# Optimization experiments

Hardware: AMD Instinct MI355X
Metric: run time of the kernel (lower is better)

Reference implementation:

```python
import jax, jax.numpy as jnp
import numpy as np
import math

HIDDEN = 768
KEY = 128      # attention_key_size
INTER = 1536   # intermediate_size
B, S = 4, 2048


def setup_inputs() -> dict:
    key = jax.random.key(0)
    ks = jax.random.split(key, 8)
    hidden_states = jax.random.normal(ks[0], (B, S, HIDDEN), dtype=jnp.float32)
    attention_mask = jax.random.randint(ks[1], (B, 1, 1, S), 0, 2, dtype=jnp.int32)
    position_ids = jnp.arange(B * S, dtype=jnp.int32).reshape(B, S) % S
    Wi = jax.random.normal(ks[2], (HIDDEN, 2 * INTER + KEY), dtype=jnp.float32) * 0.02
    bi = jnp.zeros((2 * INTER + KEY,), dtype=jnp.float32)
    gamma = jax.random.normal(ks[3], (2, KEY), dtype=jnp.float32) * 0.02 + 1.0
    beta = jnp.zeros((2, KEY), dtype=jnp.float32)
    Wo = jax.random.normal(ks[4], (INTER, HIDDEN), dtype=jnp.float32) * 0.02
    bo = jnp.zeros((HIDDEN,), dtype=jnp.float32)
    return {"hidden_states": hidden_states, "attention_mask": attention_mask,
            "position_ids": position_ids, "Wi": Wi, "bi": bi,
            "gamma": gamma, "beta": beta, "Wo": Wo, "bo": bo}


def _gau_forward(hidden_states, attention_mask, Wi, bi, gamma, beta, Wo, bo):
    # i_dense + swish activation
    h = jax.nn.silu(jnp.einsum('bsd,de->bse', hidden_states, Wi) + bi)
    u = h[..., :INTER]
    v = h[..., INTER:2 * INTER]
    qk = h[..., 2 * INTER:]
    # OffsetScale: per-head affine (heads=2 -> q, k)
    q = qk * gamma[0] + beta[0]
    k = qk * gamma[1] + beta[1]
    scores = jnp.einsum('bid,bjd->bij', q, k) / math.sqrt(KEY)
    # additive mask: (1 - m) * -1e12, squeeze head dim
    am = (1.0 - attention_mask.astype(scores.dtype)) * -1e12
    scores = scores + am[:, 0]  # [B,1,S] broadcasts over query dim
    # softmax_plus normalization: scale logits by log(l)/log(512)
    valid = (scores > -1e11).astype(scores.dtype)
    l = jnp.maximum(jnp.sum(valid, axis=-1, keepdims=True), 1.0)
    scale = jnp.log(l) / jnp.log(jnp.asarray(512.0, scores.dtype))
    attn = jax.nn.softmax(scores * scale, axis=-1)
    ctx = jnp.einsum('bij,bjd->bid', attn, v)
    return jnp.einsum('bse,eh->bsh', u * ctx, Wo) + bo


def reference(hidden_states, attention_mask, position_ids, Wi, bi, gamma, beta, Wo, bo):
    # position_ids unused: p_bias is not 'rotary'
    return _gau_forward(hidden_states, attention_mask, Wi, bi, gamma, beta, Wo, bo)
```

## Files before the change

kernel.cpp:

```cpp
#include <hip/hip_runtime.h>
#include <math.h>

#define HIDDEN 768
#define KEY    128
#define INTER  1536
#define NB     4
#define SEQ    2048
#define MTOT   (NB*SEQ)
#define ETOT   (2*INTER+KEY)
#define CS     136

typedef short bf16x8 __attribute__((ext_vector_type(8)));
typedef float f32x4  __attribute__((ext_vector_type(4)));
typedef unsigned short u16x8 __attribute__((ext_vector_type(8)));

__device__ __forceinline__ unsigned short f2bfbits(float x) {
    union { float f; unsigned int u; } a; a.f = x;
    unsigned int r = a.u + 0x7fffu + ((a.u >> 16) & 1u);
    return (unsigned short)(r >> 16);
}
__device__ __forceinline__ float bfbits2f(unsigned short b) {
    union { float f; unsigned int u; } a; a.u = ((unsigned int)b) << 16;
    return a.f;
}

__device__ __forceinline__ void gl2lds16(const unsigned short* g, unsigned short* l) {
    __builtin_amdgcn_global_load_lds(
        (const __attribute__((address_space(1))) unsigned int*)g,
        (__attribute__((address_space(3))) unsigned int*)l, 16, 0, 0);
}

__global__ __launch_bounds__(256) void scale_kernel(const int* __restrict__ mask,
                                                    float* __restrict__ scaleb) {
    __shared__ int red[256];
    int b = blockIdx.x;
    int s = 0;
    for (int j = threadIdx.x; j < SEQ; j += 256)
        s += (mask[b*SEQ + j] != 0) ? 1 : 0;
    red[threadIdx.x] = s;
    __syncthreads();
    for (int step = 128; step > 0; step >>= 1) {
        if (threadIdx.x < step) red[threadIdx.x] += red[threadIdx.x + step];
        __syncthreads();
    }
    if (threadIdx.x == 0) {
        float l = fmaxf((float)red[0], 1.0f);
        scaleb[b] = logf(l) / logf(512.0f);
    }
}

__global__ __launch_bounds__(256) void cvt_bf16_kernel(const float* __restrict__ in,
                                                       unsigned short* __restrict__ out, int n4) {
    int i = blockIdx.x*256 + threadIdx.x;
    if (i < n4) {
        float4 v = ((const float4*)in)[i];
        ushort4 o;
        o.x = f2bfbits(v.x); o.y = f2bfbits(v.y);
        o.z = f2bfbits(v.z); o.w = f2bfbits(v.w);
        ((ushort4*)out)[i] = o;
    }
}

__global__ __launch_bounds__(256) void transpose_cvt(const float* __restrict__ in,
                                                     unsigned short* __restrict__ out,
                                                     int R, int C) {
    __shared__ unsigned short tile[32][33];
    int c0 = blockIdx.x*32, r0 = blockIdx.y*32;
    int tx = threadIdx.x & 31, ty4 = (threadIdx.x >> 5)*4;
    #pragma unroll
    for (int rr = 0; rr < 4; rr++) {
        int r = ty4 + rr;
        tile[r][tx] = f2bfbits(in[(size_t)(r0+r)*C + c0+tx]);
    }
    __syncthreads();
    #pragma unroll
    for (int rr = 0; rr < 4; rr++) {
        int r = ty4 + rr;
        out[(size_t)(c0+r)*R + r0+tx] = tile[tx][r];
    }
}

__device__ __forceinline__ void mfma_core(
    const unsigned short* __restrict__ Abase, int lda,
    const unsigned short* __restrict__ Bbase, int ldb,
    unsigned short* As, unsigned short* Bs,
    f32x4 acc[4][4], int tid, int ktot)
{
    const int lane = tid & 63, wave = tid >> 6;
    const int wm = (wave >> 1) << 6, wn = (wave & 1) << 6;
    const int lm = lane & 15;
    const int q8 = (lane >> 4) << 3;
    const int row_a = tid >> 2, col_a = (tid & 3) << 3;
    const int row_b = row_a + 64;

    for (int k0 = 0; k0 < ktot; k0 += 64) {
        if (k0) __syncthreads();
        gl2lds16(Abase + (size_t)row_a*lda + k0 + col_a,        As + tid*8);
        gl2lds16(Abase + (size_t)row_b*lda + k0 + col_a,        As + (tid+256)*8);
        gl2lds16(Bbase + (size_t)row_a*ldb + k0 + col_a,        Bs + tid*8);
        gl2lds16(Bbase + (size_t)row_b*ldb + k0 + col_a,        Bs + (tid+256)*8);
        gl2lds16(Abase + (size_t)row_a*lda + k0+32 + col_a,     As + 4096 + tid*8);
        gl2lds16(Abase + (size_t)row_b*lda + k0+32 + col_a,     As + 4096 + (tid+256)*8);
        gl2lds16(Bbase + (size_t)row_a*ldb + k0+32 + col_a,     Bs + 4096 + tid*8);
        gl2lds16(Bbase + (size_t)row_b*ldb + k0+32 + col_a,     Bs + 4096 + (tid+256)*8);
        __syncthreads();
        #pragma unroll
        for (int h = 0; h < 2; h++) {
            const unsigned short* Ah = As + h*4096;
            const unsigned short* Bh = Bs + h*4096;
            bf16x8 af[4], bfr[4];
            #pragma unroll
            for (int i = 0; i < 4; i++)
                af[i] = *(const bf16x8*)&Ah[(wm + i*16 + lm)*32 + q8];
            #pragma unroll
            for (int j = 0; j < 4; j++)
                bfr[j] = *(const bf16x8*)&Bh[(wn + j*16 + lm)*32 + q8];
            #pragma unroll
            for (int i = 0; i < 4; i++)
                #pragma unroll
                for (int j = 0; j < 4; j++)
                    acc[i][j] = __builtin_amdgcn_mfma_f32_16x16x32_bf16(af[i], bfr[j], acc[i][j], 0, 0, 0);
        }
    }
}

#define EPILOG_IDX \
    const int lane = tid & 63, wave = tid >> 6; \
    const int wm = (wave >> 1) << 6, wn = (wave & 1) << 6; \
    const int cn = lane & 15, r4 = (lane >> 4) << 2;

__global__ __launch_bounds__(256) void gemm1_mfma(
    const unsigned short* __restrict__ Xb, const unsigned short* __restrict__ WiT,
    const float* __restrict__ bi, const float* __restrict__ gamma, const float* __restrict__ beta,
    unsigned short* __restrict__ u, unsigned short* __restrict__ vT,
    unsigned short* __restrict__ qb, unsigned short* __restrict__ kb)
{
    __shared__ __align__(16) unsigned short smem[128*CS];
    unsigned short* As = smem;
    unsigned short* Bs = smem + 8192;
    const int tid = threadIdx.x;
    const int row0 = blockIdx.y*128, col0 = blockIdx.x*128;
    f32x4 acc[4][4];
    #pragma unroll
    for (int i = 0; i < 4; i++)
        #pragma unroll
        for (int j = 0; j < 4; j++)
            acc[i][j] = (f32x4){0.f,0.f,0.f,0.f};
    mfma_core(Xb + (size_t)row0*HIDDEN, HIDDEN, WiT + (size_t)col0*HIDDEN, HIDDEN,
              As, Bs, acc, tid, HIDDEN);
    EPILOG_IDX
    __syncthreads();
    #pragma unroll
    for (int j = 0; j < 4; j++) {
        int nl = wn + j*16 + cn;
        float bin = bi[col0 + nl];
        #pragma unroll
        for (int i = 0; i < 4; i++) {
            #pragma unroll
            for (int r = 0; r < 4; r++) {
                int rowl = wm + i*16 + r4 + r;
                float x = acc[i][j][r] + bin;
                float h = x / (1.0f + __expf(-x));
                smem[rowl*CS + nl] = f2bfbits(h);
            }
        }
    }
    __syncthreads();
    if (col0 < INTER) {
        #pragma unroll
        for (int rnd = 0; rnd < 8; rnd++) {
            int row = rnd*16 + (tid>>4);
            int col = (tid&15)*8;
            u16x8 h = *(const u16x8*)&smem[row*CS + col];
            *(u16x8*)&u[(size_t)(row0+row)*INTER + col0 + col] = h;
        }
    } else if (col0 < 2*INTER) {
        int c = tid >> 1;
        int half = tid & 1;
        int b = row0 / SEQ;
        int srow = row0 - b*SEQ + half*64;
        size_t base = ((size_t)b*INTER + (col0 - INTER) + c)*SEQ + srow;
        #pragma unroll
        for (int k = 0; k < 8; k++) {
            u16x8 h;
            #pragma unroll
            for (int t = 0; t < 8; t++)
                h[t] = smem[(half*64 + k*8 + t)*CS + c];
            *(u16x8*)&vT[base + k*8] = h;
        }
    } else {
        #pragma unroll
        for (int rnd = 0; rnd < 8; rnd++) {
            int row = rnd*16 + (tid>>4);
            int col = (tid&15)*8;
            u16x8 h = *(const u16x8*)&smem[row*CS + col];
            int m = row0 + row;
            u16x8 qo, ko;
            #pragma unroll
            for (int t = 0; t < 8; t++) {
                float hv = bfbits2f(h[t]);
                qo[t] = f2bfbits(hv*gamma[col+t]     + beta[col+t]);
                ko[t] = f2bfbits(hv*gamma[KEY+col+t] + beta[KEY+col+t]);
            }
            *(u16x8*)&qb[(size_t)m*KEY + col] = qo;
            *(u16x8*)&kb[(size_t)m*KEY + col] = ko;
        }
    }
}

__global__ __launch_bounds__(256) void attn_mfma(
    const unsigned short* __restrict__ qb, const unsigned short* __restrict__ kb,
    const int* __restrict__ mask, const float* __restrict__ scaleb,
    unsigned short* __restrict__ P)
{
    __shared__ __align__(16) unsigned short smem[128*CS];
    unsigned short* As = smem;
    unsigned short* Bs = smem + 8192;
    const int tid = threadIdx.x;
    const int z = blockIdx.z;
    const int row0 = blockIdx.y*128, col0 = blockIdx.x*128;
    f32x4 acc[4][4];
    #pragma unroll
    for (int i = 0; i < 4; i++)
        #pragma unroll
        for (int j = 0; j < 4; j++)
            acc[i][j] = (f32x4){0.f,0.f,0.f,0.f};
    mfma_core(qb + ((size_t)z*SEQ + row0)*KEY, KEY, kb + ((size_t)z*SEQ + col0)*KEY, KEY,
              As, Bs, acc, tid, KEY);
    const float st = scaleb[z] * 0.08838834764831845f;
    EPILOG_IDX
    __syncthreads();
    #pragma unroll
    for (int j = 0; j < 4; j++) {
        int nl = wn + j*16 + cn;
        float mkf = (mask[z*SEQ + col0 + nl] != 0) ? 1.0f : 0.0f;
        #pragma unroll
        for (int i = 0; i < 4; i++) {
            #pragma unroll
            for (int r = 0; r < 4; r++) {
                int rowl = wm + i*16 + r4 + r;
                float p = mkf * __expf(acc[i][j][r]*st);
                smem[rowl*CS + nl] = f2bfbits(p);
            }
        }
    }
    __syncthreads();
    #pragma unroll
    for (int rnd = 0; rnd < 8; rnd++) {
        int row = rnd*16 + (tid>>4);
        int col = (tid&15)*8;
        u16x8 h = *(const u16x8*)&smem[row*CS + col];
        *(u16x8*)&P[((size_t)z*SEQ + row0 + row)*SEQ + col0 + col] = h;
    }
}

__global__ __launch_bounds__(256) void rowsum_kernel(const unsigned short* __restrict__ P,
                                                     float* __restrict__ lbuf) {
    int row = blockIdx.x*4 + (threadIdx.x >> 6);
    int lane = threadIdx.x & 63;
    const unsigned short* pr = P + (size_t)row*SEQ;
    float s = 0.f;
    for (int c = lane*8; c < SEQ; c += 64*8) {
        ushort4 a = *(const ushort4*)&pr[c];
        ushort4 b = *(const ushort4*)&pr[c+4];
        s += bfbits2f(a.x)+bfbits2f(a.y)+bfbits2f(a.z)+bfbits2f(a.w)
           + bfbits2f(b.x)+bfbits2f(b.y)+bfbits2f(b.z)+bfbits2f(b.w);
    }
    #pragma unroll
    for (int off = 32; off > 0; off >>= 1) s += __shfl_down(s, off, 64);
    if (lane == 0) lbuf[row] = s;
}

__global__ __launch_bounds__(256) void pv_mfma(
    const unsigned short* __restrict__ P, const unsigned short* __restrict__ vT,
    const float* __restrict__ lbuf, unsigned short* __restrict__ u)
{
    __shared__ __align__(16) unsigned short smem[128*CS];
    unsigned short* As = smem;
    unsigned short* Bs = smem + 8192;
    const int tid = threadIdx.x;
    const int z = blockIdx.z;
    const int row0 = blockIdx.y*128, col0 = blockIdx.x*128;
    f32x4 acc[4][4];
    #pragma unroll
    for (int i = 0; i < 4; i++)
        #pragma unroll
        for (int j = 0; j < 4; j++)
            acc[i][j] = (f32x4){0.f,0.f,0.f,0.f};
    mfma_core(P + ((size_t)z*SEQ + row0)*SEQ, SEQ, vT + ((size_t)z*INTER + col0)*SEQ, SEQ,
              As, Bs, acc, tid, SEQ);
    EPILOG_IDX
    __syncthreads();
    #pragma unroll
    for (int j = 0; j < 4; j++) {
        int nl = wn + j*16 + cn;
        #pragma unroll
        for (int i = 0; i < 4; i++) {
            #pragma unroll
            for (int r = 0; r < 4; r++) {
                int rowl = wm + i*16 + r4 + r;
                smem[rowl*CS + nl] = f2bfbits(acc[i][j][r]);
            }
        }
    }
    __syncthreads();
    #pragma unroll
    for (int rnd = 0; rnd < 8; rnd++) {
        int row = rnd*16 + (tid>>4);
        int col = (tid&15)*8;
        int m = z*SEQ + row0 + row;
        float linv = 1.0f / lbuf[m];
        u16x8 cx = *(const u16x8*)&smem[row*CS + col];
        size_t idx = (size_t)m*INTER + col0 + col;
        u16x8 uu = *(const u16x8*)&u[idx];
        u16x8 g;
        #pragma unroll
        for (int t = 0; t < 8; t++)
            g[t] = f2bfbits(bfbits2f(uu[t]) * bfbits2f(cx[t]) * linv);
        *(u16x8*)&u[idx] = g;
    }
}

__global__ __launch_bounds__(256) void gemm2_mfma(
    const unsigned short* __restrict__ g, const unsigned short* __restrict__ WoT,
    const float* __restrict__ bo, float* __restrict__ out)
{
    __shared__ __align__(16) unsigned short As[8192];
    __shared__ __align__(16) unsigned short Bs[8192];
    const int tid = threadIdx.x;
    const int row0 = blockIdx.y*128, col0 = blockIdx.x*128;
    f32x4 acc[4][4];
    #pragma unroll
    for (int i = 0; i < 4; i++)
        #pragma unroll
        for (int j = 0; j < 4; j++)
            acc[i][j] = (f32x4){0.f,0.f,0.f,0.f};
    mfma_core(g + (size_t)row0*INTER, INTER, WoT + (size_t)col0*INTER, INTER,
              As, Bs, acc, tid, INTER);
    EPILOG_IDX
    #pragma unroll
    for (int j = 0; j < 4; j++) {
        int n = col0 + wn + j*16 + cn;
        float bon = bo[n];
        #pragma unroll
        for (int i = 0; i < 4; i++) {
            #pragma unroll
            for (int r = 0; r < 4; r++) {
                int m = row0 + wm + i*16 + r4 + r;
                out[(size_t)m*HIDDEN + n] = acc[i][j][r] + bon;
            }
        }
    }
}

extern "C" void kernel_launch(void* const* d_in, const int* in_sizes, int n_in,
                              void* d_out, int out_size, void* d_ws, size_t ws_size,
                              hipStream_t stream)
{
    const float* X     = (const float*)d_in[0];
    const int*   mask  = (const int*)d_in[1];
    const float* Wi    = (const float*)d_in[3];
    const float* bi    = (const float*)d_in[4];
    const float* gamma = (const float*)d_in[5];
    const float* beta  = (const float*)d_in[6];
    const float* Wo    = (const float*)d_in[7];
    const float* bo    = (const float*)d_in[8];
    float* out = (float*)d_out;

    unsigned short* Xb  = (unsigned short*)d_ws;
    unsigned short* WiT = Xb  + (size_t)MTOT*HIDDEN;
    unsigned short* WoT = WiT + (size_t)ETOT*HIDDEN;
    unsigned short* u   = WoT + (size_t)HIDDEN*INTER;
    unsigned short* vT  = u   + (size_t)MTOT*INTER;
    unsigned short* qb  = vT  + (size_t)MTOT*INTER;
    unsigned short* kb  = qb  + (size_t)MTOT*KEY;
    unsigned short* P   = kb  + (size_t)MTOT*KEY;
    float* lb  = (float*)(P + (size_t)NB*SEQ*SEQ);
    float* scb = lb + MTOT;

    scale_kernel<<<NB, 256, 0, stream>>>(mask, scb);
    cvt_bf16_kernel<<<(MTOT*HIDDEN/4 + 255)/256, 256, 0, stream>>>(X, Xb, MTOT*HIDDEN/4);
    transpose_cvt<<<dim3(ETOT/32, HIDDEN/32), 256, 0, stream>>>(Wi, WiT, HIDDEN, ETOT);
    transpose_cvt<<<dim3(HIDDEN/32, INTER/32), 256, 0, stream>>>(Wo, WoT, INTER, HIDDEN);
    gemm1_mfma<<<dim3(ETOT/128, MTOT/128), 256, 0, stream>>>(Xb, WiT, bi, gamma, beta, u, vT, qb, kb);
    attn_mfma<<<dim3(SEQ/128, SEQ/128, NB), 256, 0, stream>>>(qb, kb, mask, scb, P);
    rowsum_kernel<<<MTOT/4, 256, 0, stream>>>(P, lb);
    pv_mfma<<<dim3(INTER/128, SEQ/128, NB), 256, 0, stream>>>(P, vT, lb, u);
    gemm2_mfma<<<dim3(HIDDEN/128, MTOT/128), 256, 0, stream>>>(u, WoT, bo, out);
}
```

Before: 301.9 us.

## Fuse rowsum into attention, split-K gemm2, and shrink K-tile for GEMMs

Removes the separate rowsum kernel: the attention kernel sums each bf16 P row fragment, reduces across 16 lanes and atomically adds into a zeroed lbuf. gemm2 is split along K into two halves written to a partial buffer that reuses the P region, and a combine kernel adds the halves plus the bias. mfma_core is templated on K-tile size, with BK=32 for gemm1 and gemm2 to cut LDS use and raise occupancy. The cost is float atomics whose order is nondeterministic, an extra memset and kernel launch, and extra fp32 partial-buffer traffic.

```diff
diff --git a/kernel.cpp b/kernel.cpp
--- a/kernel.cpp
+++ b/kernel.cpp
@@ -80,6 +80,7 @@
     }
 }
 
+template<int BK>
 __device__ __forceinline__ void mfma_core(
     const unsigned short* __restrict__ Abase, int lda,
     const unsigned short* __restrict__ Bbase, int ldb,
@@ -93,19 +94,18 @@
     const int row_a = tid >> 2, col_a = (tid & 3) << 3;
     const int row_b = row_a + 64;
 
-    for (int k0 = 0; k0 < ktot; k0 += 64) {
+    for (int k0 = 0; k0 < ktot; k0 += BK) {
         if (k0) __syncthreads();
-        gl2lds16(Abase + (size_t)row_a*lda + k0 + col_a,        As + tid*8);
-        gl2lds16(Abase + (size_t)row_b*lda + k0 + col_a,        As + (tid+256)*8);
-        gl2lds16(Bbase + (size_t)row_a*ldb + k0 + col_a,        Bs + tid*8);
-        gl2lds16(Bbase + (size_t)row_b*ldb + k0 + col_a,        Bs + (tid+256)*8);
-        gl2lds16(Abase + (size_t)row_a*lda + k0+32 + col_a,     As + 4096 + tid*8);
-        gl2lds16(Abase + (size_t)row_b*lda + k0+32 + col_a,     As + 4096 + (tid+256)*8);
-        gl2lds16(Bbase + (size_t)row_a*ldb + k0+32 + col_a,     Bs + 4096 + tid*8);
-        gl2lds16(Bbase + (size_t)row_b*ldb + k0+32 + col_a,     Bs + 4096 + (tid+256)*8);
+        #pragma unroll
+        for (int h = 0; h < BK/32; h++) {
+            gl2lds16(Abase + (size_t)row_a*lda + k0 + h*32 + col_a, As + h*4096 + tid*8);
+            gl2lds16(Abase + (size_t)row_b*lda + k0 + h*32 + col_a, As + h*4096 + (tid+256)*8);
+            gl2lds16(Bbase + (size_t)row_a*ldb + k0 + h*32 + col_a, Bs + h*4096 + tid*8);
+            gl2lds16(Bbase + (size_t)row_b*ldb + k0 + h*32 + col_a, Bs + h*4096 + (tid+256)*8);
+        }
         __syncthreads();
         #pragma unroll
-        for (int h = 0; h < 2; h++) {
+        for (int h = 0; h < BK/32; h++) {
             const unsigned short* Ah = As + h*4096;
             const unsigned short* Bh = Bs + h*4096;
             bf16x8 af[4], bfr[4];
@@ -137,7 +137,7 @@
 {
     __shared__ __align__(16) unsigned short smem[128*CS];
     unsigned short* As = smem;
-    unsigned short* Bs = smem + 8192;
+    unsigned short* Bs = smem + 4096;
     const int tid = threadIdx.x;
     const int row0 = blockIdx.y*128, col0 = blockIdx.x*128;
     f32x4 acc[4][4];
@@ -146,8 +146,8 @@
         #pragma unroll
         for (int j = 0; j < 4; j++)
             acc[i][j] = (f32x4){0.f,0.f,0.f,0.f};
-    mfma_core(Xb + (size_t)row0*HIDDEN, HIDDEN, WiT + (size_t)col0*HIDDEN, HIDDEN,
-              As, Bs, acc, tid, HIDDEN);
+    mfma_core<32>(Xb + (size_t)row0*HIDDEN, HIDDEN, WiT + (size_t)col0*HIDDEN, HIDDEN,
+                  As, Bs, acc, tid, HIDDEN);
     EPILOG_IDX
     __syncthreads();
     #pragma unroll
@@ -211,7 +211,7 @@
 __global__ __launch_bounds__(256) void attn_mfma(
     const unsigned short* __restrict__ qb, const unsigned short* __restrict__ kb,
     const int* __restrict__ mask, const float* __restrict__ scaleb,
-    unsigned short* __restrict__ P)
+    unsigned short* __restrict__ P, float* __restrict__ lbuf)
 {
     __shared__ __align__(16) unsigned short smem[128*CS];
     unsigned short* As = smem;
@@ -225,8 +225,8 @@
         #pragma unroll
         for (int j = 0; j < 4; j++)
             acc[i][j] = (f32x4){0.f,0.f,0.f,0.f};
-    mfma_core(qb + ((size_t)z*SEQ + row0)*KEY, KEY, kb + ((size_t)z*SEQ + col0)*KEY, KEY,
-              As, Bs, acc, tid, KEY);
+    mfma_core<64>(qb + ((size_t)z*SEQ + row0)*KEY, KEY, kb + ((size_t)z*SEQ + col0)*KEY, KEY,
+                  As, Bs, acc, tid, KEY);
     const float st = scaleb[z] * 0.08838834764831845f;
     EPILOG_IDX
     __syncthreads();
@@ -251,24 +251,14 @@
         int col = (tid&15)*8;
         u16x8 h = *(const u16x8*)&smem[row*CS + col];
         *(u16x8*)&P[((size_t)z*SEQ + row0 + row)*SEQ + col0 + col] = h;
-    }
-}
-
-__global__ __launch_bounds__(256) void rowsum_kernel(const unsigned short* __restrict__ P,
-                                                     float* __restrict__ lbuf) {
-    int row = blockIdx.x*4 + (threadIdx.x >> 6);
-    int lane = threadIdx.x & 63;
-    const unsigned short* pr = P + (size_t)row*SEQ;
-    float s = 0.f;
-    for (int c = lane*8; c < SEQ; c += 64*8) {
-        ushort4 a = *(const ushort4*)&pr[c];
-        ushort4 b = *(const ushort4*)&pr[c+4];
-        s += bfbits2f(a.x)+bfbits2f(a.y)+bfbits2f(a.z)+bfbits2f(a.w)
-           + bfbits2f(b.x)+bfbits2f(b.y)+bfbits2f(b.z)+bfbits2f(b.w);
-    }
-    #pragma unroll
-    for (int off = 32; off > 0; off >>= 1) s += __shfl_down(s, off, 64);
-    if (lane == 0) lbuf[row] = s;
+        float s8 = 0.f;
+        #pragma unroll
+        for (int t = 0; t < 8; t++) s8 += bfbits2f(h[t]);
+        #pragma unroll
+        for (int off = 8; off > 0; off >>= 1) s8 += __shfl_xor(s8, off, 16);
+        if ((tid & 15) == 0)
+            atomicAdd(&lbuf[z*SEQ + row0 + row], s8);
+    }
 }
 
 __global__ __launch_bounds__(256) void pv_mfma(
@@ -287,8 +277,8 @@
         #pragma unroll
         for (int j = 0; j < 4; j++)
             acc[i][j] = (f32x4){0.f,0.f,0.f,0.f};
-    mfma_core(P + ((size_t)z*SEQ + row0)*SEQ, SEQ, vT + ((size_t)z*INTER + col0)*SEQ, SEQ,
-              As, Bs, acc, tid, SEQ);
+    mfma_core<64>(P + ((size_t)z*SEQ + row0)*SEQ, SEQ, vT + ((size_t)z*INTER + col0)*SEQ, SEQ,
+                  As, Bs, acc, tid, SEQ);
     EPILOG_IDX
     __syncthreads();
     #pragma unroll
@@ -321,13 +311,14 @@
     }
 }
 
-__global__ __launch_bounds__(256) void gemm2_mfma(
+__global__ __launch_bounds__(256) void gemm2_part(
     const unsigned short* __restrict__ g, const unsigned short* __restrict__ WoT,
-    const float* __restrict__ bo, float* __restrict__ out)
-{
-    __shared__ __align__(16) unsigned short As[8192];
-    __shared__ __align__(16) unsigned short Bs[8192];
+    float* __restrict__ part)
+{
+    __shared__ __align__(16) unsigned short As[4096];
+    __shared__ __align__(16) unsigned short Bs[4096];
     const int tid = threadIdx.x;
+    const int z = blockIdx.z;
     const int row0 = blockIdx.y*128, col0 = blockIdx.x*128;
     f32x4 acc[4][4];
     #pragma unroll
@@ -335,22 +326,38 @@
         #pragma unroll
         for (int j = 0; j < 4; j++)
             acc[i][j] = (f32x4){0.f,0.f,0.f,0.f};
-    mfma_core(g + (size_t)row0*INTER, INTER, WoT + (size_t)col0*INTER, INTER,
-              As, Bs, acc, tid, INTER);
+    mfma_core<32>(g + (size_t)row0*INTER + z*768, INTER,
+                  WoT + (size_t)col0*INTER + z*768, INTER,
+                  As, Bs, acc, tid, 768);
+    float* dst = part + (size_t)z*MTOT*HIDDEN;
     EPILOG_IDX
     #pragma unroll
     for (int j = 0; j < 4; j++) {
         int n = col0 + wn + j*16 + cn;
-        float bon = bo[n];
         #pragma unroll
         for (int i = 0; i < 4; i++) {
             #pragma unroll
             for (int r = 0; r < 4; r++) {
                 int m = row0 + wm + i*16 + r4 + r;
-                out[(size_t)m*HIDDEN + n] = acc[i][j][r] + bon;
-            }
-        }
-    }
+                dst[(size_t)m*HIDDEN + n] = acc[i][j][r];
+            }
+        }
+    }
+}
+
+__global__ __launch_bounds__(256) void gemm2_combine(
+    const float* __restrict__ part, const float* __restrict__ bo,
+    float* __restrict__ out)
+{
+    int i = blockIdx.x*256 + threadIdx.x;
+    const float4* p0 = (const float4*)part;
+    const float4* p1 = (const float4*)(part + (size_t)MTOT*HIDDEN);
+    int n = (i*4) % HIDDEN;
+    float4 a = p0[i], b = p1[i], c = *(const float4*)&bo[n];
+    float4 o;
+    o.x = a.x + b.x + c.x; o.y = a.y + b.y + c.y;
+    o.z = a.z + b.z + c.z; o.w = a.w + b.w + c.w;
+    ((float4*)out)[i] = o;
 }
 
 extern "C" void kernel_launch(void* const* d_in, const int* in_sizes, int n_in,
@@ -375,16 +382,18 @@
     unsigned short* qb  = vT  + (size_t)MTOT*INTER;
     unsigned short* kb  = qb  + (size_t)MTOT*KEY;
     unsigned short* P   = kb  + (size_t)MTOT*KEY;
+    float* part = (float*)P;
     float* lb  = (float*)(P + (size_t)NB*SEQ*SEQ);
     float* scb = lb + MTOT;
 
+    hipMemsetAsync(lb, 0, MTOT*sizeof(float), stream);
     scale_kernel<<<NB, 256, 0, stream>>>(mask, scb);
     cvt_bf16_kernel<<<(MTOT*HIDDEN/4 + 255)/256, 256, 0, stream>>>(X, Xb, MTOT*HIDDEN/4);
     transpose_cvt<<<dim3(ETOT/32, HIDDEN/32), 256, 0, stream>>>(Wi, WiT, HIDDEN, ETOT);
     transpose_cvt<<<dim3(HIDDEN/32, INTER/32), 256, 0, stream>>>(Wo, WoT, INTER, HIDDEN);
     gemm1_mfma<<<dim3(ETOT/128, MTOT/128), 256, 0, stream>>>(Xb, WiT, bi, gamma, beta, u, vT, qb, kb);
-    attn_mfma<<<dim3(SEQ/128, SEQ/128, NB), 256, 0, stream>>>(qb, kb, mask, scb, P);
-    rowsum_kernel<<<MTOT/4, 256, 0, stream>>>(P, lb);
+    attn_mfma<<<dim3(SEQ/128, SEQ/128, NB), 256, 0, stream>>>(qb, kb, mask, scb, P, lb);
     pv_mfma<<<dim3(INTER/128, SEQ/128, NB), 256, 0, stream>>>(P, vT, lb, u);
-    gemm2_mfma<<<dim3(HIDDEN/128, MTOT/128), 256, 0, stream>>>(u, WoT, bo, out);
-}
+    gemm2_part<<<dim3(HIDDEN/128, MTOT/128, 2), 256, 0, stream>>>(u, WoT, part);
+    gemm2_combine<<<MTOT*HIDDEN/4/256, 256, 0, stream>>>(part, bo, out);
+}
```

After: 321.1 us. +6.3%, slower.

## Remap GEMM blocks to XCD-aware tile order and template K-step size

Applied to the files above, without the earlier changes.

Replaces the 2D/3D grids of gemm1, pv and gemm2 with a 1D grid whose block index is decoded so that consecutive blocks dispatched to the same XCD cover neighbouring output tiles, aiming to improve L2 reuse of shared A/B panels. mfma_core is templated on the K step, and gemm1 now uses a 32-wide step, which halves its LDS footprint for A/B. The smaller K step adds more barriers per tile in gemm1. The hardcoded decoding depends on the exact tile counts being divisible by 8.

```diff
diff --git a/kernel.cpp b/kernel.cpp
--- a/kernel.cpp
+++ b/kernel.cpp
@@ -80,6 +80,7 @@
     }
 }
 
+template<int BK>
 __device__ __forceinline__ void mfma_core(
     const unsigned short* __restrict__ Abase, int lda,
     const unsigned short* __restrict__ Bbase, int ldb,
@@ -93,19 +94,18 @@
     const int row_a = tid >> 2, col_a = (tid & 3) << 3;
     const int row_b = row_a + 64;
 
-    for (int k0 = 0; k0 < ktot; k0 += 64) {
+    for (int k0 = 0; k0 < ktot; k0 += BK) {
         if (k0) __syncthreads();
-        gl2lds16(Abase + (size_t)row_a*lda + k0 + col_a,        As + tid*8);
-        gl2lds16(Abase + (size_t)row_b*lda + k0 + col_a,        As + (tid+256)*8);
-        gl2lds16(Bbase + (size_t)row_a*ldb + k0 + col_a,        Bs + tid*8);
-        gl2lds16(Bbase + (size_t)row_b*ldb + k0 + col_a,        Bs + (tid+256)*8);
-        gl2lds16(Abase + (size_t)row_a*lda + k0+32 + col_a,     As + 4096 + tid*8);
-        gl2lds16(Abase + (size_t)row_b*lda + k0+32 + col_a,     As + 4096 + (tid+256)*8);
-        gl2lds16(Bbase + (size_t)row_a*ldb + k0+32 + col_a,     Bs + 4096 + tid*8);
-        gl2lds16(Bbase + (size_t)row_b*ldb + k0+32 + col_a,     Bs + 4096 + (tid+256)*8);
+        #pragma unroll
+        for (int h = 0; h < BK/32; h++) {
+            gl2lds16(Abase + (size_t)row_a*lda + k0 + h*32 + col_a, As + h*4096 + tid*8);
+            gl2lds16(Abase + (size_t)row_b*lda + k0 + h*32 + col_a, As + h*4096 + (tid+256)*8);
+            gl2lds16(Bbase + (size_t)row_a*ldb + k0 + h*32 + col_a, Bs + h*4096 + tid*8);
+            gl2lds16(Bbase + (size_t)row_b*ldb + k0 + h*32 + col_a, Bs + h*4096 + (tid+256)*8);
+        }
         __syncthreads();
         #pragma unroll
-        for (int h = 0; h < 2; h++) {
+        for (int h = 0; h < BK/32; h++) {
             const unsigned short* Ah = As + h*4096;
             const unsigned short* Bh = Bs + h*4096;
             bf16x8 af[4], bfr[4];
@@ -137,17 +137,21 @@
 {
     __shared__ __align__(16) unsigned short smem[128*CS];
     unsigned short* As = smem;
-    unsigned short* Bs = smem + 8192;
+    unsigned short* Bs = smem + 4096;
     const int tid = threadIdx.x;
-    const int row0 = blockIdx.y*128, col0 = blockIdx.x*128;
+    const int bid = blockIdx.x;
+    const int xcd = bid & 7, slot = bid >> 3;
+    const int xt = slot >> 3;
+    const int yt = (xcd << 3) + (slot & 7);
+    const int row0 = yt*128, col0 = xt*128;
     f32x4 acc[4][4];
     #pragma unroll
     for (int i = 0; i < 4; i++)
         #pragma unroll
         for (int j = 0; j < 4; j++)
             acc[i][j] = (f32x4){0.f,0.f,0.f,0.f};
-    mfma_core(Xb + (size_t)row0*HIDDEN, HIDDEN, WiT + (size_t)col0*HIDDEN, HIDDEN,
-              As, Bs, acc, tid, HIDDEN);
+    mfma_core<32>(Xb + (size_t)row0*HIDDEN, HIDDEN, WiT + (size_t)col0*HIDDEN, HIDDEN,
+                  As, Bs, acc, tid, HIDDEN);
     EPILOG_IDX
     __syncthreads();
     #pragma unroll
@@ -225,8 +229,8 @@
         #pragma unroll
         for (int j = 0; j < 4; j++)
             acc[i][j] = (f32x4){0.f,0.f,0.f,0.f};
-    mfma_core(qb + ((size_t)z*SEQ + row0)*KEY, KEY, kb + ((size_t)z*SEQ + col0)*KEY, KEY,
-              As, Bs, acc, tid, KEY);
+    mfma_core<64>(qb + ((size_t)z*SEQ + row0)*KEY, KEY, kb + ((size_t)z*SEQ + col0)*KEY, KEY,
+                  As, Bs, acc, tid, KEY);
     const float st = scaleb[z] * 0.08838834764831845f;
     EPILOG_IDX
     __syncthreads();
@@ -279,16 +283,20 @@
     unsigned short* As = smem;
     unsigned short* Bs = smem + 8192;
     const int tid = threadIdx.x;
-    const int z = blockIdx.z;
-    const int row0 = blockIdx.y*128, col0 = blockIdx.x*128;
+    const int bid = blockIdx.x;
+    const int xcd = bid & 7, slot = bid >> 3;
+    const int z = slot / 24, pos = slot % 24;
+    const int yt = (xcd & 3)*4 + pos/6;
+    const int xt = (xcd >> 2)*6 + pos%6;
+    const int row0 = yt*128, col0 = xt*128;
     f32x4 acc[4][4];
     #pragma unroll
     for (int i = 0; i < 4; i++)
         #pragma unroll
         for (int j = 0; j < 4; j++)
             acc[i][j] = (f32x4){0.f,0.f,0.f,0.f};
-    mfma_core(P + ((size_t)z*SEQ + row0)*SEQ, SEQ, vT + ((size_t)z*INTER + col0)*SEQ, SEQ,
-              As, Bs, acc, tid, SEQ);
+    mfma_core<64>(P + ((size_t)z*SEQ + row0)*SEQ, SEQ, vT + ((size_t)z*INTER + col0)*SEQ, SEQ,
+                  As, Bs, acc, tid, SEQ);
     EPILOG_IDX
     __syncthreads();
     #pragma unroll
@@ -328,15 +336,19 @@
     __shared__ __align__(16) unsigned short As[8192];
     __shared__ __align__(16) unsigned short Bs[8192];
     const int tid = threadIdx.x;
-    const int row0 = blockIdx.y*128, col0 = blockIdx.x*128;
+    const int bid = blockIdx.x;
+    const int xcd = bid & 7, slot = bid >> 3;
+    const int xt = slot >> 3;
+    const int yt = (xcd << 3) + (slot & 7);
+    const int row0 = yt*128, col0 = xt*128;
     f32x4 acc[4][4];
     #pragma unroll
     for (int i = 0; i < 4; i++)
         #pragma unroll
         for (int j = 0; j < 4; j++)
             acc[i][j] = (f32x4){0.f,0.f,0.f,0.f};
-    mfma_core(g + (size_t)row0*INTER, INTER, WoT + (size_t)col0*INTER, INTER,
-              As, Bs, acc, tid, INTER);
+    mfma_core<64>(g + (size_t)row0*INTER, INTER, WoT + (size_t)col0*INTER, INTER,
+                  As, Bs, acc, tid, INTER);
     EPILOG_IDX
     #pragma unroll
     for (int j = 0; j < 4; j++) {
@@ -382,9 +394,9 @@
     cvt_bf16_kernel<<<(MTOT*HIDDEN/4 + 255)/256, 256, 0, stream>>>(X, Xb, MTOT*HIDDEN/4);
     transpose_cvt<<<dim3(ETOT/32, HIDDEN/32), 256, 0, stream>>>(Wi, WiT, HIDDEN, ETOT);
     transpose_cvt<<<dim3(HIDDEN/32, INTER/32), 256, 0, stream>>>(Wo, WoT, INTER, HIDDEN);
-    gemm1_mfma<<<dim3(ETOT/128, MTOT/128), 256, 0, stream>>>(Xb, WiT, bi, gamma, beta, u, vT, qb, kb);
+    gemm1_mfma<<<1600, 256, 0, stream>>>(Xb, WiT, bi, gamma, beta, u, vT, qb, kb);
     attn_mfma<<<dim3(SEQ/128, SEQ/128, NB), 256, 0, stream>>>(qb, kb, mask, scb, P);
     rowsum_kernel<<<MTOT/4, 256, 0, stream>>>(P, lb);
-    pv_mfma<<<dim3(INTER/128, SEQ/128, NB), 256, 0, stream>>>(P, vT, lb, u);
-    gemm2_mfma<<<dim3(HIDDEN/128, MTOT/128), 256, 0, stream>>>(u, WoT, bo, out);
-}
+    pv_mfma<<<768, 256, 0, stream>>>(P, vT, lb, u);
+    gemm2_mfma<<<384, 256, 0, stream>>>(u, WoT, bo, out);
+}
```

Result: no change. 302.3 us (+0.1%).
